# Performance work log

Hardware: AMD Instinct MI355X
Metric: run time of the kernel (lower is better)

Reference implementation:

```python
import jax, jax.numpy as jnp
import numpy as np

B, SQ, SKV, E, H = 4, 2048, 2048, 1024, 16
HD = E // H  # 64


def stablemax(x):
    # StableMax: s(x) = x+1 if x>=0 else 1/(1-x), normalized along last axis
    s = jnp.where(x >= 0, x + 1.0, 1.0 / (1.0 - x))
    return s / jnp.sum(s, axis=-1, keepdims=True)


def setup_inputs() -> dict:
    key = jax.random.key(0)
    ks = jax.random.split(key, 6)
    scale = 1.0 / np.sqrt(E)
    return {
        "query": jax.random.normal(ks[0], (B, SQ, E), jnp.float32),
        "key_value": jax.random.normal(ks[1], (B, SKV, E), jnp.float32),
        "Wq": jax.random.normal(ks[2], (E, E), jnp.float32) * scale,
        "bq": jnp.zeros((E,), jnp.float32),
        "Wk": jax.random.normal(ks[3], (E, E), jnp.float32) * scale,
        "bk": jnp.zeros((E,), jnp.float32),
        "Wv": jax.random.normal(ks[4], (E, E), jnp.float32) * scale,
        "bv": jnp.zeros((E,), jnp.float32),
        "Wo": jax.random.normal(ks[5], (E, E), jnp.float32) * scale,
        "bo": jnp.zeros((E,), jnp.float32),
    }


def reference(query, key_value, Wq, bq, Wk, bk, Wv, bv, Wo, bo):
    b = query.shape[0]
    # linear projections (torch Linear: x @ W^T + b)
    q = query @ Wq.T + bq
    k = key_value @ Wk.T + bk
    v = key_value @ Wv.T + bv
    # [B, H, S, HD]
    q = q.reshape(b, -1, H, HD).transpose(0, 2, 1, 3)
    k = k.reshape(b, -1, H, HD).transpose(0, 2, 1, 3)
    v = v.reshape(b, -1, H, HD).transpose(0, 2, 1, 3)
    scores = jnp.einsum("bhqd,bhkd->bhqk", q, k) / np.sqrt(HD).astype(np.float32)
    attn = stablemax(scores)  # dropout is identity in eval mode
    context = jnp.einsum("bhqk,bhkd->bhqd", attn, v)
    context = context.transpose(0, 2, 1, 3).reshape(b, -1, E)
    return context @ Wo.T + bo
```

## Files before the change

kernel.cpp:

```cpp
#include <hip/hip_runtime.h>

typedef __bf16 bf16;
typedef __bf16 bf16x8 __attribute__((ext_vector_type(8)));
typedef __bf16 bf16x4 __attribute__((ext_vector_type(4)));
typedef _Float16 f16;
typedef _Float16 f16x2 __attribute__((ext_vector_type(2)));
typedef _Float16 f16x4 __attribute__((ext_vector_type(4)));
typedef float f32x4 __attribute__((ext_vector_type(4)));

__device__ __forceinline__ f32x4 mfma_qk(bf16x8 a, bf16x8 b, f32x4 c) {
    return __builtin_amdgcn_mfma_f32_16x16x32_bf16(a, b, c, 0, 0, 0);
}
__device__ __forceinline__ f32x4 mfma_pv(f16x4 a, f16x4 b, f32x4 c) {
    return __builtin_amdgcn_mfma_f32_16x16x16f16(a, b, c, 0, 0, 0);
}

#define GLOAD_LDS16(gp, lp)                                                    \
    __builtin_amdgcn_global_load_lds(                                          \
        (const __attribute__((address_space(1))) unsigned int*)(gp),           \
        (__attribute__((address_space(3))) unsigned int*)(lp), 16, 0, 0)

__global__ __launch_bounds__(256) void cast_inputs(
    const float* __restrict__ w0, const float* __restrict__ w1,
    const float* __restrict__ w2, const float* __restrict__ w3,
    const float* __restrict__ kv, const float* __restrict__ q,
    bf16* __restrict__ Wb, bf16* __restrict__ KVa, bf16* __restrict__ Qb) {
    long i4 = (long)blockIdx.x * 256 + threadIdx.x;
    const float* src;
    bf16* dst;
    long loc;
    if (i4 < 1048576) {
        int which = (int)(i4 >> 18);
        loc = (i4 & 262143) << 2;
        src = which == 0 ? w0 : which == 1 ? w1 : which == 2 ? w2 : w3;
        dst = Wb + ((long)which << 20);
    } else if (i4 < 3145728) {
        loc = (i4 - 1048576) << 2;
        src = kv; dst = KVa;
    } else {
        loc = (i4 - 3145728) << 2;
        src = q; dst = Qb;
    }
    float4 f = *(const float4*)(src + loc);
    bf16x4 o;
    o[0] = (bf16)f.x; o[1] = (bf16)f.y; o[2] = (bf16)f.z; o[3] = (bf16)f.w;
    *(bf16x4*)(dst + loc) = o;
}

__device__ __forceinline__ void gemm_core(
    const bf16* __restrict__ A, const bf16* __restrict__ Wt,
    const float* __restrict__ bias, void* __restrict__ Yv,
    const int om, bf16* smem, const int n0, const int m0) {
    constexpr int Kd = 1024, Nd = 1024;
    constexpr int TP = 132;
    bf16* As = smem;
    bf16* Bs = smem + 8192;
    const int tid = threadIdx.x;
    const int wid = tid >> 6, lane = tid & 63;
    const int l16 = lane & 15, quad = lane >> 4;
    const int mh = (wid >> 1) * 64, nh = (wid & 1) * 64;

    f32x4 acc[4][4];
#pragma unroll
    for (int i = 0; i < 4; ++i)
#pragma unroll
        for (int j = 0; j < 4; ++j) acc[i][j] = (f32x4){0.f, 0.f, 0.f, 0.f};

    for (int k0 = 0; k0 < Kd; k0 += 64) {
#pragma unroll
        for (int j = 0; j < 4; ++j) {
            const int s = j * 256 + tid;
            const int r = s >> 3, c8 = (s & 7) ^ (r & 7);
            GLOAD_LDS16(A + (long)(m0 + r) * Kd + k0 + c8 * 8, &As[s * 8]);
            GLOAD_LDS16(Wt + (long)(n0 + r) * Kd + k0 + c8 * 8, &Bs[s * 8]);
        }
        __syncthreads();
#pragma unroll
        for (int kc = 0; kc < 2; ++kc) {
            bf16x8 af[4], bq[4];
#pragma unroll
            for (int i = 0; i < 4; ++i) {
                const int row = mh + i * 16 + l16;
                af[i] = *(const bf16x8*)&As[(row * 8 + ((kc * 4 + quad) ^ (row & 7))) * 8];
            }
#pragma unroll
            for (int i = 0; i < 4; ++i) {
                const int row = nh + i * 16 + l16;
                bq[i] = *(const bf16x8*)&Bs[(row * 8 + ((kc * 4 + quad) ^ (row & 7))) * 8];
            }
#pragma unroll
            for (int i = 0; i < 4; ++i)
#pragma unroll
                for (int j = 0; j < 4; ++j)
                    acc[i][j] = mfma_qk(af[i], bq[j], acc[i][j]);
        }
        __syncthreads();
    }

    if (om == 2) {
#pragma unroll
        for (int j = 0; j < 4; ++j) {
            const int col = nh + j * 16 + l16;
            const float bv = bias[n0 + col];
#pragma unroll
            for (int i = 0; i < 4; ++i)
#pragma unroll
                for (int p = 0; p < 2; ++p) {
                    f16x2 pk2;
                    pk2[0] = (f16)(acc[i][j][p * 2 + 0] + bv);
                    pk2[1] = (f16)(acc[i][j][p * 2 + 1] + bv);
                    *(f16x2*)&smem[col * TP + mh + i * 16 + quad * 4 + p * 2] = pk2;
                }
        }
        __syncthreads();
        const int b_ = m0 >> 11, skv0 = m0 & 2047;
        const int rowc = tid & 15;
#pragma unroll
        for (int c = 0; c < 8; ++c) {
            const int col = (tid >> 4) + c * 16;
            const int colg = n0 + col;
            bf16x8 v = *(const bf16x8*)&smem[col * TP + rowc * 8];
            const long base = ((long)((b_ * 16 + (colg >> 6)) * 64 + (colg & 63))) << 11;
            *(bf16x8*)((bf16*)Yv + base + skv0 + rowc * 8) = v;
        }
    } else {
#pragma unroll
        for (int j = 0; j < 4; ++j) {
            const int col = n0 + nh + j * 16 + l16;
            const float bv = bias[col];
#pragma unroll
            for (int i = 0; i < 4; ++i)
#pragma unroll
                for (int r = 0; r < 4; ++r) {
                    int row = m0 + mh + i * 16 + quad * 4 + r;
                    float v = acc[i][j][r] + bv;
                    if (om == 1)
                        ((float*)Yv)[(long)row * Nd + col] = v;
                    else
                        ((bf16*)Yv)[(long)row * Nd + col] = (bf16)v;
                }
        }
    }
}

__global__ __launch_bounds__(256) void proj_q(
    const bf16* __restrict__ Qb, const bf16* __restrict__ Wq,
    const float* __restrict__ bq, bf16* __restrict__ Qw) {
    __shared__ __align__(16) bf16 smem[16896];
    gemm_core(Qb, Wq, bq, Qw, 0, smem, blockIdx.x * 128, blockIdx.y * 128);
}

__global__ __launch_bounds__(256) void proj_kv(
    const bf16* __restrict__ KVa,
    const bf16* __restrict__ Wk, const float* __restrict__ bk, bf16* __restrict__ Kw,
    const bf16* __restrict__ Wv, const float* __restrict__ bv, f16* __restrict__ Vt) {
    __shared__ __align__(16) bf16 smem[16896];
    if (blockIdx.z == 0)
        gemm_core(KVa, Wk, bk, Kw, 0, smem, blockIdx.x * 128, blockIdx.y * 128);
    else
        gemm_core(KVa, Wv, bv, Vt, 2, smem, blockIdx.x * 128, blockIdx.y * 128);
}

__global__ __launch_bounds__(256) void gemm_o(
    const bf16* __restrict__ Cw, const bf16* __restrict__ Wo,
    const float* __restrict__ bo, float* __restrict__ out) {
    __shared__ __align__(16) bf16 smem[16896];
    gemm_core(Cw, Wo, bo, out, 1, smem, blockIdx.x * 128, blockIdx.y * 128);
}

__global__ __launch_bounds__(256) void attn_kernel(
    const bf16* __restrict__ Q, const bf16* __restrict__ K,
    const f16* __restrict__ Vt, bf16* __restrict__ C) {
    constexpr int E = 1024, S = 2048;
    __shared__ __align__(16) char smem_raw[32768];
    bf16* Ks = (bf16*)smem_raw;
    f16* VTs = (f16*)(smem_raw + 16384);

    const int tid = threadIdx.x;
    const int wid = tid >> 6, lane = tid & 63;
    const int l16 = lane & 15, quad = lane >> 4;
    const int qt = blockIdx.x, h = blockIdx.y, b = blockIdx.z;

    const long q0 = (long)b * S + qt * 128;
    const bf16* Qg = Q + q0 * E + h * 64;
    const bf16* Kg = K + (long)b * S * E + h * 64;
    const f16* Vg = Vt + ((long)(b * 16 + h) << 17);

    bf16x8 qf[2][2];
#pragma unroll
    for (int mt = 0; mt < 2; ++mt)
#pragma unroll
        for (int kc = 0; kc < 2; ++kc)
            qf[mt][kc] = *(const bf16x8*)(Qg + (long)(wid * 32 + mt * 16 + l16) * E + kc * 32 + quad * 8);

    f32x4 ctx[2][4];
    float den[2] = {0.f, 0.f};
#pragma unroll
    for (int mt = 0; mt < 2; ++mt)
#pragma unroll
        for (int dt = 0; dt < 4; ++dt) ctx[mt][dt] = (f32x4){0.f, 0.f, 0.f, 0.f};

    for (int kv0 = 0; kv0 < S; kv0 += 128) {
#pragma unroll
        for (int j = 0; j < 4; ++j) {
            const int s = j * 256 + tid;
            const int r = s >> 3, c8 = (s & 7) ^ (r & 7);
            GLOAD_LDS16(Kg + (long)(kv0 + r) * E + c8 * 8, &Ks[s * 8]);
        }
#pragma unroll
        for (int j = 0; j < 4; ++j) {
            const int s = j * 256 + tid;
            const int r = s >> 4, c16 = (s & 15) ^ (r & 15);
            GLOAD_LDS16(Vg + (long)r * S + kv0 + c16 * 8, &VTs[s * 8]);
        }
        __syncthreads();

#pragma unroll
        for (int kvm = 0; kvm < 8; ++kvm) {
            const int rk = kvm * 16 + l16, rb = rk & 7;
            bf16x8 kf0 = *(const bf16x8*)&Ks[(rk * 8 + (quad ^ rb)) * 8];
            bf16x8 kf1 = *(const bf16x8*)&Ks[(rk * 8 + ((quad + 4) ^ rb)) * 8];

            f16x4 pp[2];
#pragma unroll
            for (int mt = 0; mt < 2; ++mt) {
                f32x4 sacc = mfma_qk(kf0, qf[mt][0], (f32x4){0.f, 0.f, 0.f, 0.f});
                sacc = mfma_qk(kf1, qf[mt][1], sacc);
#pragma unroll
                for (int r = 0; r < 4; ++r) {
                    float x = sacc[r];
                    float u = __builtin_fmaf(__builtin_fabsf(x), 0.125f, 1.0f);
                    float sv = (x >= 0.f) ? u : __builtin_amdgcn_rcpf(u);
                    den[mt] += sv;
                    pp[mt][r] = (f16)sv;
                }
            }
            const int c16 = 2 * kvm + (quad >> 1);
            const int ho = (quad & 1) * 4;
#pragma unroll
            for (int dt = 0; dt < 4; ++dt) {
                const int rv = dt * 16 + l16;
                f16x4 vf = *(const f16x4*)&VTs[(rv * 16 + (c16 ^ l16)) * 8 + ho];
#pragma unroll
                for (int mt = 0; mt < 2; ++mt)
                    ctx[mt][dt] = mfma_pv(vf, pp[mt], ctx[mt][dt]);
            }
        }
        __syncthreads();
    }

    float scl[2];
#pragma unroll
    for (int mt = 0; mt < 2; ++mt) {
        float d = den[mt];
        d += __shfl_xor(d, 16);
        d += __shfl_xor(d, 32);
        scl[mt] = __builtin_amdgcn_rcpf(d);
    }

    bf16* Os = (bf16*)smem_raw;
#pragma unroll
    for (int mt = 0; mt < 2; ++mt)
#pragma unroll
        for (int dt = 0; dt < 4; ++dt) {
            bf16x4 o;
#pragma unroll
            for (int r = 0; r < 4; ++r) o[r] = (bf16)(ctx[mt][dt][r] * scl[mt]);
            *(bf16x4*)&Os[(wid * 32 + mt * 16 + l16) * 68 + dt * 16 + quad * 4] = o;
        }
    __syncthreads();
    {
        const int r = tid >> 1, c = (tid & 1) * 32;
        bf16* cp = C + (q0 + r) * E + h * 64 + c;
#pragma unroll
        for (int j = 0; j < 4; ++j)
            *(bf16x8*)(cp + j * 8) = *(const bf16x8*)&Os[r * 68 + c + j * 8];
    }
}

extern "C" void kernel_launch(void* const* d_in, const int* in_sizes, int n_in,
                              void* d_out, int out_size, void* d_ws, size_t ws_size,
                              hipStream_t stream) {
    const float* query = (const float*)d_in[0];
    const float* keyv  = (const float*)d_in[1];
    const float* Wq = (const float*)d_in[2];
    const float* bq = (const float*)d_in[3];
    const float* Wk = (const float*)d_in[4];
    const float* bk = (const float*)d_in[5];
    const float* Wv = (const float*)d_in[6];
    const float* bv = (const float*)d_in[7];
    const float* Wo = (const float*)d_in[8];
    const float* bo = (const float*)d_in[9];

    char* ws = (char*)d_ws;
    bf16* Wb  = (bf16*)ws;
    bf16* KVa = (bf16*)(ws + (8l << 20));
    bf16* Qb  = (bf16*)(ws + (24l << 20));
    bf16* Qw  = (bf16*)(ws + (40l << 20));
    f16*  Vt  = (f16*)(ws + (56l << 20));
    bf16* Kw  = Qb;
    bf16* Cw  = KVa;

    cast_inputs<<<20480, 256, 0, stream>>>(Wq, Wk, Wv, Wo, keyv, query, Wb, KVa, Qb);

    dim3 gg(8, 64);
    proj_q<<<gg, 256, 0, stream>>>(Qb, Wb, bq, Qw);
    proj_kv<<<dim3(8, 64, 2), 256, 0, stream>>>(KVa, Wb + (1l << 20), bk, Kw,
                                                Wb + (2l << 20), bv, Vt);

    attn_kernel<<<dim3(16, 16, 4), 256, 0, stream>>>(Qw, Kw, Vt, Cw);

    gemm_o<<<gg, 256, 0, stream>>>(Cw, Wb + (3l << 20), bo, (float*)d_out);
}
```

Before: 347.9 us.

## Merge QKV projections, remap blocks per XCD, use 16x16x32 f16 MFMA for PV

Combines the Q and KV projection kernels into a single launch of 1536 blocks. This one launch, gemm_o and attention all remap block IDs so that neighbouring tiles land on the same XCD, aiming for better L2 reuse. The attention inner loop now handles 32 KV columns per step using the wider 16x16x32 f16 MFMA, places s_setprio around the MFMA groups, and adds a launch-bounds occupancy hint. K is stored in the output buffer, which frees workspace but depends on gemm_o running after attention has finished reading it.

```diff
diff --git a/kernel.cpp b/kernel.cpp
--- a/kernel.cpp
+++ b/kernel.cpp
@@ -6,13 +6,14 @@
 typedef _Float16 f16;
 typedef _Float16 f16x2 __attribute__((ext_vector_type(2)));
 typedef _Float16 f16x4 __attribute__((ext_vector_type(4)));
+typedef _Float16 f16x8 __attribute__((ext_vector_type(8)));
 typedef float f32x4 __attribute__((ext_vector_type(4)));
 
 __device__ __forceinline__ f32x4 mfma_qk(bf16x8 a, bf16x8 b, f32x4 c) {
     return __builtin_amdgcn_mfma_f32_16x16x32_bf16(a, b, c, 0, 0, 0);
 }
-__device__ __forceinline__ f32x4 mfma_pv(f16x4 a, f16x4 b, f32x4 c) {
-    return __builtin_amdgcn_mfma_f32_16x16x16f16(a, b, c, 0, 0, 0);
+__device__ __forceinline__ f32x4 mfma_pv32(f16x8 a, f16x8 b, f32x4 c) {
+    return __builtin_amdgcn_mfma_f32_16x16x32_f16(a, b, c, 0, 0, 0);
 }
 
 #define GLOAD_LDS16(gp, lp)                                                    \
@@ -143,32 +144,35 @@
     }
 }
 
-__global__ __launch_bounds__(256) void proj_q(
-    const bf16* __restrict__ Qb, const bf16* __restrict__ Wq,
-    const float* __restrict__ bq, bf16* __restrict__ Qw) {
+__global__ __launch_bounds__(256) void proj_qkv(
+    const bf16* __restrict__ Qb, const bf16* __restrict__ KVa,
+    const bf16* __restrict__ Wb,
+    const float* __restrict__ bq, const float* __restrict__ bk,
+    const float* __restrict__ bv,
+    bf16* __restrict__ Qw, bf16* __restrict__ Kw, f16* __restrict__ Vt) {
     __shared__ __align__(16) bf16 smem[16896];
-    gemm_core(Qb, Wq, bq, Qw, 0, smem, blockIdx.x * 128, blockIdx.y * 128);
-}
-
-__global__ __launch_bounds__(256) void proj_kv(
-    const bf16* __restrict__ KVa,
-    const bf16* __restrict__ Wk, const float* __restrict__ bk, bf16* __restrict__ Kw,
-    const bf16* __restrict__ Wv, const float* __restrict__ bv, f16* __restrict__ Vt) {
-    __shared__ __align__(16) bf16 smem[16896];
-    if (blockIdx.z == 0)
-        gemm_core(KVa, Wk, bk, Kw, 0, smem, blockIdx.x * 128, blockIdx.y * 128);
+    const int lin = blockIdx.x + (blockIdx.y << 3) + (blockIdx.z << 9);
+    const int nid = (lin & 7) * 192 + (lin >> 3);
+    const int z = nid >> 9, rem = nid & 511;
+    const int n0 = (rem & 7) << 7, m0 = (rem >> 3) << 7;
+    if (z == 0)
+        gemm_core(Qb, Wb, bq, Qw, 0, smem, n0, m0);
+    else if (z == 1)
+        gemm_core(KVa, Wb + (1l << 20), bk, Kw, 0, smem, n0, m0);
     else
-        gemm_core(KVa, Wv, bv, Vt, 2, smem, blockIdx.x * 128, blockIdx.y * 128);
+        gemm_core(KVa, Wb + (2l << 20), bv, Vt, 2, smem, n0, m0);
 }
 
 __global__ __launch_bounds__(256) void gemm_o(
     const bf16* __restrict__ Cw, const bf16* __restrict__ Wo,
     const float* __restrict__ bo, float* __restrict__ out) {
     __shared__ __align__(16) bf16 smem[16896];
-    gemm_core(Cw, Wo, bo, out, 1, smem, blockIdx.x * 128, blockIdx.y * 128);
-}
-
-__global__ __launch_bounds__(256) void attn_kernel(
+    const int lin = blockIdx.x + (blockIdx.y << 3);
+    const int nid = (lin & 7) * 64 + (lin >> 3);
+    gemm_core(Cw, Wo, bo, out, 1, smem, (nid & 7) << 7, (nid >> 3) << 7);
+}
+
+__global__ __launch_bounds__(256, 4) void attn_kernel(
     const bf16* __restrict__ Q, const bf16* __restrict__ K,
     const f16* __restrict__ Vt, bf16* __restrict__ C) {
     constexpr int E = 1024, S = 2048;
@@ -179,7 +183,9 @@
     const int tid = threadIdx.x;
     const int wid = tid >> 6, lane = tid & 63;
     const int l16 = lane & 15, quad = lane >> 4;
-    const int qt = blockIdx.x, h = blockIdx.y, b = blockIdx.z;
+    const int lin = blockIdx.x + (blockIdx.y << 4) + (blockIdx.z << 8);
+    const int nid = (lin & 7) * 128 + (lin >> 3);
+    const int qt = nid & 15, h = (nid >> 4) & 15, b = nid >> 8;
 
     const long q0 = (long)b * S + qt * 128;
     const bf16* Qg = Q + q0 * E + h * 64;
@@ -216,34 +222,49 @@
         __syncthreads();
 
 #pragma unroll
-        for (int kvm = 0; kvm < 8; ++kvm) {
-            const int rk = kvm * 16 + l16, rb = rk & 7;
-            bf16x8 kf0 = *(const bf16x8*)&Ks[(rk * 8 + (quad ^ rb)) * 8];
-            bf16x8 kf1 = *(const bf16x8*)&Ks[(rk * 8 + ((quad + 4) ^ rb)) * 8];
-
-            f16x4 pp[2];
+        for (int kvp = 0; kvp < 4; ++kvp) {
+            f32x4 sacc[2][2];
+#pragma unroll
+            for (int s = 0; s < 2; ++s) {
+                const int rk = kvp * 32 + s * 16 + l16, rb = rk & 7;
+                bf16x8 kf0 = *(const bf16x8*)&Ks[(rk * 8 + (quad ^ rb)) * 8];
+                bf16x8 kf1 = *(const bf16x8*)&Ks[(rk * 8 + ((quad + 4) ^ rb)) * 8];
+                __builtin_amdgcn_s_setprio(1);
+#pragma unroll
+                for (int mt = 0; mt < 2; ++mt) {
+                    f32x4 t = mfma_qk(kf0, qf[mt][0], (f32x4){0.f, 0.f, 0.f, 0.f});
+                    sacc[s][mt] = mfma_qk(kf1, qf[mt][1], t);
+                }
+                __builtin_amdgcn_s_setprio(0);
+            }
+            f16x8 pp[2];
 #pragma unroll
             for (int mt = 0; mt < 2; ++mt) {
-                f32x4 sacc = mfma_qk(kf0, qf[mt][0], (f32x4){0.f, 0.f, 0.f, 0.f});
-                sacc = mfma_qk(kf1, qf[mt][1], sacc);
-#pragma unroll
-                for (int r = 0; r < 4; ++r) {
-                    float x = sacc[r];
-                    float u = __builtin_fmaf(__builtin_fabsf(x), 0.125f, 1.0f);
-                    float sv = (x >= 0.f) ? u : __builtin_amdgcn_rcpf(u);
-                    den[mt] += sv;
-                    pp[mt][r] = (f16)sv;
+#pragma unroll
+                for (int s = 0; s < 2; ++s) {
+                    float sv[4];
+#pragma unroll
+                    for (int r = 0; r < 4; ++r) {
+                        float x = sacc[s][mt][r];
+                        float u = __builtin_fmaf(__builtin_fabsf(x), 0.125f, 1.0f);
+                        sv[r] = (x >= 0.f) ? u : __builtin_amdgcn_rcpf(u);
+                        pp[mt][s * 4 + r] = (f16)sv[r];
+                    }
+                    den[mt] += (sv[0] + sv[1]) + (sv[2] + sv[3]);
                 }
             }
-            const int c16 = 2 * kvm + (quad >> 1);
-            const int ho = (quad & 1) * 4;
+            const int c16l = 4 * kvp + (quad >> 1), ho = (quad & 1) * 4;
 #pragma unroll
             for (int dt = 0; dt < 4; ++dt) {
                 const int rv = dt * 16 + l16;
-                f16x4 vf = *(const f16x4*)&VTs[(rv * 16 + (c16 ^ l16)) * 8 + ho];
+                f16x4 vlo = *(const f16x4*)&VTs[(rv * 16 + (c16l ^ l16)) * 8 + ho];
+                f16x4 vhi = *(const f16x4*)&VTs[(rv * 16 + ((c16l + 2) ^ l16)) * 8 + ho];
+                f16x8 vf = __builtin_shufflevector(vlo, vhi, 0, 1, 2, 3, 4, 5, 6, 7);
+                __builtin_amdgcn_s_setprio(1);
 #pragma unroll
                 for (int mt = 0; mt < 2; ++mt)
-                    ctx[mt][dt] = mfma_pv(vf, pp[mt], ctx[mt][dt]);
+                    ctx[mt][dt] = mfma_pv32(vf, pp[mt], ctx[mt][dt]);
+                __builtin_amdgcn_s_setprio(0);
             }
         }
         __syncthreads();
@@ -298,17 +319,14 @@
     bf16* Qb  = (bf16*)(ws + (24l << 20));
     bf16* Qw  = (bf16*)(ws + (40l << 20));
     f16*  Vt  = (f16*)(ws + (56l << 20));
-    bf16* Kw  = Qb;
+    bf16* Kw  = (bf16*)d_out;
     bf16* Cw  = KVa;
 
     cast_inputs<<<20480, 256, 0, stream>>>(Wq, Wk, Wv, Wo, keyv, query, Wb, KVa, Qb);
 
-    dim3 gg(8, 64);
-    proj_q<<<gg, 256, 0, stream>>>(Qb, Wb, bq, Qw);
-    proj_kv<<<dim3(8, 64, 2), 256, 0, stream>>>(KVa, Wb + (1l << 20), bk, Kw,
-                                                Wb + (2l << 20), bv, Vt);
+    proj_qkv<<<dim3(8, 64, 3), 256, 0, stream>>>(Qb, KVa, Wb, bq, bk, bv, Qw, Kw, Vt);
 
     attn_kernel<<<dim3(16, 16, 4), 256, 0, stream>>>(Qw, Kw, Vt, Cw);
 
-    gemm_o<<<gg, 256, 0, stream>>>(Cw, Wb + (3l << 20), bo, (float*)d_out);
-}
+    gemm_o<<<dim3(8, 64), 256, 0, stream>>>(Cw, Wb + (3l << 20), bo, (float*)d_out);
+}
```

New measurement: 771.4 us. 122% more time.
